# Kernel tuning notes

Hardware: AMD Instinct MI355X
Metric: run time of the kernel (lower is better)

The kernel has to match this reference:

```python
import jax, jax.numpy as jnp
import numpy as np

B, N, F_IN, H, E, C = 64, 1024, 128, 128, 1048576, 6
RATIO = 0.5
N1 = int(N * RATIO)        # nodes per graph after pool1 = 512
N2 = int(N1 * RATIO)       # nodes per graph after pool2 = 256


def setup_inputs() -> dict:
    key = jax.random.key(0)
    ks = jax.random.split(key, 14)
    x = jax.random.normal(ks[0], (B * N, F_IN), jnp.float32)
    # edges constrained within each graph (uniform graph size N)
    src = jax.random.randint(ks[1], (E,), 0, B * N, dtype=jnp.int32)
    dst = (src // N) * N + jax.random.randint(ks[2], (E,), 0, N, dtype=jnp.int32)
    edge_index = jnp.stack([src, dst]).astype(jnp.int64)
    batch = jnp.repeat(jnp.arange(B, dtype=jnp.int64), N)

    def lin(k, i, o):
        return (jax.random.normal(k, (i, o), jnp.float32) / np.sqrt(i)).astype(jnp.float32)

    W1 = lin(ks[3], F_IN, H); b1 = jnp.zeros((H,), jnp.float32)
    ws1 = jax.random.normal(ks[4], (H,), jnp.float32) / np.sqrt(H)
    W2 = lin(ks[5], H, H); b2 = jnp.zeros((H,), jnp.float32)
    ws2 = jax.random.normal(ks[6], (H,), jnp.float32) / np.sqrt(H)
    W3 = lin(ks[7], H, H); b3 = jnp.zeros((H,), jnp.float32)
    ws3 = jax.random.normal(ks[8], (H,), jnp.float32) / np.sqrt(H)
    L1w = lin(ks[9], 2 * H, H); L1b = jnp.zeros((H,), jnp.float32)
    L2w = lin(ks[10], H, H // 2); L2b = jnp.zeros((H // 2,), jnp.float32)
    L3w = lin(ks[11], H // 2, C); L3b = jnp.zeros((C,), jnp.float32)
    return dict(x=x, edge_index=edge_index, batch=batch,
                W1=W1, b1=b1, ws1=ws1, W2=W2, b2=b2, ws2=ws2, W3=W3, b3=b3, ws3=ws3,
                L1w=L1w, L1b=L1b, L2w=L2w, L2b=L2b, L3w=L3w, L3b=L3b)


def gcn_conv(x, src, dst, emask, W, b, ws, n_nodes):
    # GCNConv with self-loops: out_i = sum_j m_ij h_j / sqrt(d_i d_j) + h_i / d_i, d = deg+1
    h = x @ W
    deg = jax.ops.segment_sum(emask, dst, num_segments=n_nodes) + 1.0
    norm = emask / jnp.sqrt(deg[src] * deg[dst])                 # [E]
    agg = jax.ops.segment_sum(h[src] * norm[:, None], dst, num_segments=n_nodes)
    out = agg + h / deg[:, None] + b
    score = out @ ws                                             # [n] attention score
    return out, score


def att_pool(x, score, src, dst, emask, n_per_graph):
    # top-k node selection per graph (uniform sizes -> static shapes)
    k = int(n_per_graph * RATIO)
    vals, idx = jax.lax.top_k(score.reshape(B, n_per_graph), k)  # [B, k]
    gidx = (idx + (jnp.arange(B) * n_per_graph)[:, None]).reshape(-1)
    x_new = x[gidx] * jnp.tanh(vals.reshape(-1))[:, None]
    # remap old node ids -> new compact ids; drop edges touching removed nodes
    newpos = jnp.full((B * n_per_graph,), -1, jnp.int32).at[gidx].set(
        jnp.arange(B * k, dtype=jnp.int32))
    nsrc = newpos[src]; ndst = newpos[dst]
    nmask = emask * (nsrc >= 0) * (ndst >= 0)
    return x_new, jnp.maximum(nsrc, 0), jnp.maximum(ndst, 0), nmask, k


def readout(h, bvec, n_per_graph):
    gmp = jax.ops.segment_max(h, bvec, num_segments=B)
    gap = jax.ops.segment_sum(h, bvec, num_segments=B) / n_per_graph
    return jnp.concatenate([gmp, gap], axis=1)                   # [B, 2H]


def reference(x, edge_index, batch, W1, b1, ws1, W2, b2, ws2, W3, b3, ws3,
              L1w, L1b, L2w, L2b, L3w, L3b):
    src = edge_index[0].astype(jnp.int32)
    dst = edge_index[1].astype(jnp.int32)
    emask = jnp.ones((E,), x.dtype)

    h, s = gcn_conv(x, src, dst, emask, W1, b1, ws1, B * N)
    h = jax.nn.relu(h)
    h, src, dst, emask, k1 = att_pool(h, s, src, dst, emask, N)
    b1v = jnp.repeat(jnp.arange(B), k1)
    x1 = readout(h, b1v, float(k1))

    h, s = gcn_conv(h, src, dst, emask, W2, b2, ws2, B * k1)
    h = jax.nn.relu(h)
    h, src, dst, emask, k2 = att_pool(h, s, src, dst, emask, k1)
    b2v = jnp.repeat(jnp.arange(B), k2)
    x2 = readout(h, b2v, float(k2))

    h, s = gcn_conv(h, src, dst, emask, W3, b3, ws3, B * k2)
    h = jax.nn.relu(h)
    x3 = readout(h, b2v, float(k2))

    z = jax.nn.relu(x1) + jax.nn.relu(x2) + jax.nn.relu(x3)
    z = jax.nn.relu(z @ L1w + L1b)
    z = jax.nn.relu(z @ L2w + L2b)
    return jax.nn.log_softmax(z @ L3w + L3b, axis=-1)
```

## Files before the change

kernel.cpp:

```cpp
#include <hip/hip_runtime.h>
#include <math.h>

#define E_TOT 1048576
#define NB    64
#define HD    128
#define NN1   65536
#define NN2   32768
#define NN3   16384
#define CAP   18432
#define WST   140
#define PSTR  64

__global__ void probe_kernel(const int* __restrict__ ei, int* __restrict__ flag,
                             int* __restrict__ gcur) {
    int t = threadIdx.x;
    if (t < 64) gcur[t] = 0;
    if (blockIdx.x == 0 && t == 0) {
        int w = 1;
        for (int i = 1; i < 64; i += 2) if (ei[i] != 0) { w = 0; break; }
        *flag = w;
    }
}

__global__ __launch_bounds__(256) void bin_pack_kernel(const int* __restrict__ ei,
                                                       const int* __restrict__ wflag,
                                                       int* __restrict__ bins,
                                                       int* __restrict__ gcur) {
    __shared__ int hist[64];
    __shared__ int base[64];
    __shared__ int gpos[64];
    __shared__ int stage[4096];
    const int t = threadIdx.x;
    const int wide = *wflag;
    const int e0 = blockIdx.x * 4096;
    const int2* ei2 = (const int2*)ei;

    int pk[16];
    #pragma unroll
    for (int j = 0; j < 16; ++j) {
        int e = e0 + j * 256 + t;
        int s, d;
        if (wide) { s = ei2[e].x; d = ei2[E_TOT + e].x; }
        else      { s = ei[e];    d = ei[E_TOT + e]; }
        int g = d >> 10;
        pk[j] = (g << 20) | ((d & 1023) << 10) | (s & 1023);
    }
    if (t < 64) hist[t] = 0;
    __syncthreads();
    #pragma unroll
    for (int j = 0; j < 16; ++j) atomicAdd(&hist[pk[j] >> 20], 1);
    __syncthreads();
    if (t < 64) {
        int v = hist[t];
        int inc = v;
        #pragma unroll
        for (int d = 1; d < 64; d <<= 1) { int u = __shfl_up(inc, d); if (t >= d) inc += u; }
        base[t] = inc - v;
        gpos[t] = atomicAdd(&gcur[t], v);
    }
    __syncthreads();
    if (t < 64) hist[t] = base[t];
    __syncthreads();
    #pragma unroll
    for (int j = 0; j < 16; ++j) {
        int p = atomicAdd(&hist[pk[j] >> 20], 1);
        stage[p] = pk[j];
    }
    __syncthreads();
    #pragma unroll
    for (int j = 0; j < 16; ++j) {
        int i = j * 256 + t;
        int v = stage[i];
        int g = v >> 20;
        int dst = gpos[g] + (i - base[g]);
        if (dst < CAP) bins[g * CAP + dst] = v;
    }
}

__global__ __launch_bounds__(1024) void graph_csr_kernel(const int* __restrict__ bins,
                                                         const int* __restrict__ gcur,
                                                         int2* __restrict__ off2,
                                                         float* __restrict__ rs,
                                                         int* __restrict__ csr) {
    __shared__ int deg[1024];
    __shared__ int cur[1024];
    __shared__ int wsum[16];
    __shared__ int ebase_s;
    const int g = blockIdx.x, t = threadIdx.x;
    const int lane = t & 63, wv = t >> 6;

    if (t < 64) {
        int v = gcur[t];
        int inc = v;
        #pragma unroll
        for (int d = 1; d < 64; d <<= 1) { int u = __shfl_up(inc, d); if (t >= d) inc += u; }
        if (t == g) ebase_s = inc - v;
    }
    deg[t] = 0;
    __syncthreads();
    const int cnt = gcur[g];
    const int ebase = ebase_s;
    const int* bin = bins + g * CAP;

    for (int i = t; i < cnt; i += 1024)
        atomicAdd(&deg[(bin[i] >> 10) & 1023], 1);
    __syncthreads();

    int dv = deg[t];
    int inc = dv;
    #pragma unroll
    for (int d = 1; d < 64; d <<= 1) { int u = __shfl_up(inc, d); if (lane >= d) inc += u; }
    if (lane == 63) wsum[wv] = inc;
    __syncthreads();
    if (t < 16) {
        int v = wsum[t];
        int inc2 = v;
        #pragma unroll
        for (int d = 1; d < 16; d <<= 1) { int u = __shfl_up(inc2, d); if (t >= d) inc2 += u; }
        wsum[t] = inc2 - v;
    }
    __syncthreads();
    int ex = inc - dv + wsum[wv];
    int beg = ebase + ex;
    off2[g * 1024 + t] = make_int2(beg, beg + dv);
    rs[g * 1024 + t]   = rsqrtf((float)(dv + 1));
    cur[t] = ex;
    __syncthreads();

    for (int i = t; i < cnt; i += 1024) {
        int v = bin[i];
        int p = atomicAdd(&cur[(v >> 10) & 1023], 1);
        csr[ebase + p] = (g << 10) + (v & 1023);
    }
}

__global__ __launch_bounds__(256) void csr_build_kernel(const int2* __restrict__ old_off2,
                                                        const int* __restrict__ old_deg,
                                                        const int* __restrict__ old_csr,
                                                        const int* __restrict__ map,
                                                        const int* __restrict__ sel,
                                                        int* __restrict__ new_csr,
                                                        int* __restrict__ deg,
                                                        float* __restrict__ rs, int nnew) {
    int wid  = (blockIdx.x * blockDim.x + threadIdx.x) >> 6;
    int lane = threadIdx.x & 63;
    if (wid >= nnew) return;
    int old = sel[wid];
    int beg, end;
    if (old_off2) { int2 oe = old_off2[old]; beg = oe.x; end = oe.y; }
    else          { beg = old * PSTR; end = beg + old_deg[old]; }
    int out = wid * PSTR;
    int total = 0;
    for (int base = beg; base < end; base += 64) {
        int i = base + lane;
        int ns = -1;
        if (i < end) ns = map[old_csr[i]];
        unsigned long long b = __ballot(ns >= 0);
        int pos = __popcll(b & ((1ULL << lane) - 1));
        if (ns >= 0 && total + pos < PSTR) new_csr[out + total + pos] = ns;
        total += __popcll(b);
    }
    if (total > PSTR) total = PSTR;
    if (lane == 0) {
        deg[wid] = total;
        rs[wid]  = rsqrtf((float)(total + 1));
    }
}

__global__ __launch_bounds__(256) void gemm_tiled_kernel(const float* __restrict__ X,
                                                         const float* __restrict__ W,
                                                         float* __restrict__ Y) {
    __shared__ float sXT[2][16][128];
    __shared__ float sW[2][16][WST];
    const int t = threadIdx.x;
    const long long row0 = (long long)blockIdx.x * 128;
    const int r0 = (t >> 4) << 3;
    const int c0 = (t & 15) << 3;
    const int wofs = c0 + ((c0 >> 5) << 2);
    const int lm  = t >> 1;
    const int lk  = (t & 1) << 3;
    const int wk  = t >> 4;
    const int wc8 = (t & 15) << 3;
    const int wpos = wc8 + ((wc8 >> 5) << 2);

    float acc[8][8];
    #pragma unroll
    for (int i = 0; i < 8; ++i)
        #pragma unroll
        for (int j = 0; j < 8; ++j) acc[i][j] = 0.f;

    {
        float4 xa = *(const float4*)(X + (row0 + lm) * 128 + lk);
        float4 xb = *(const float4*)(X + (row0 + lm) * 128 + lk + 4);
        float4 wa = *(const float4*)(W + wk * 128 + wc8);
        float4 wb = *(const float4*)(W + wk * 128 + wc8 + 4);
        sXT[0][lk + 0][lm] = xa.x; sXT[0][lk + 1][lm] = xa.y;
        sXT[0][lk + 2][lm] = xa.z; sXT[0][lk + 3][lm] = xa.w;
        sXT[0][lk + 4][lm] = xb.x; sXT[0][lk + 5][lm] = xb.y;
        sXT[0][lk + 6][lm] = xb.z; sXT[0][lk + 7][lm] = xb.w;
        *(float4*)&sW[0][wk][wpos]     = wa;
        *(float4*)&sW[0][wk][wpos + 4] = wb;
    }
    int cur = 0;
    for (int k0 = 0; k0 < 128; k0 += 16) {
        __syncthreads();
        const bool hasNext = (k0 + 16) < 128;
        float4 nxa, nxb, nwa, nwb;
        if (hasNext) {
            nxa = *(const float4*)(X + (row0 + lm) * 128 + k0 + 16 + lk);
            nxb = *(const float4*)(X + (row0 + lm) * 128 + k0 + 16 + lk + 4);
            nwa = *(const float4*)(W + (k0 + 16 + wk) * 128 + wc8);
            nwb = *(const float4*)(W + (k0 + 16 + wk) * 128 + wc8 + 4);
        }
        #pragma unroll
        for (int kk = 0; kk < 16; ++kk) {
            float4 xa = *(const float4*)&sXT[cur][kk][r0];
            float4 xb = *(const float4*)&sXT[cur][kk][r0 + 4];
            float4 wa = *(const float4*)&sW[cur][kk][wofs];
            float4 wb = *(const float4*)&sW[cur][kk][wofs + 4];
            float xr[8]  = {xa.x, xa.y, xa.z, xa.w, xb.x, xb.y, xb.z, xb.w};
            float wcv[8] = {wa.x, wa.y, wa.z, wa.w, wb.x, wb.y, wb.z, wb.w};
            #pragma unroll
            for (int i = 0; i < 8; ++i)
                #pragma unroll
                for (int j = 0; j < 8; ++j)
                    acc[i][j] = fmaf(xr[i], wcv[j], acc[i][j]);
        }
        if (hasNext) {
            int nxt = cur ^ 1;
            sXT[nxt][lk + 0][lm] = nxa.x; sXT[nxt][lk + 1][lm] = nxa.y;
            sXT[nxt][lk + 2][lm] = nxa.z; sXT[nxt][lk + 3][lm] = nxa.w;
            sXT[nxt][lk + 4][lm] = nxb.x; sXT[nxt][lk + 5][lm] = nxb.y;
            sXT[nxt][lk + 6][lm] = nxb.z; sXT[nxt][lk + 7][lm] = nxb.w;
            *(float4*)&sW[nxt][wk][wpos]     = nwa;
            *(float4*)&sW[nxt][wk][wpos + 4] = nwb;
            cur = nxt;
        }
    }

    #pragma unroll
    for (int i = 0; i < 8; ++i) {
        float* yp = Y + (row0 + r0 + i) * 128 + c0;
        float4 o0; o0.x = acc[i][0]; o0.y = acc[i][1]; o0.z = acc[i][2]; o0.w = acc[i][3];
        float4 o1; o1.x = acc[i][4]; o1.y = acc[i][5]; o1.z = acc[i][6]; o1.w = acc[i][7];
        *(float4*)yp       = o0;
        *(float4*)(yp + 4) = o1;
    }
}

__global__ __launch_bounds__(256) void gemm_gather_kernel(const float* __restrict__ H,
                                                          const int* __restrict__ sel,
                                                          const float* __restrict__ scal,
                                                          const float* __restrict__ W,
                                                          float* __restrict__ Y) {
    __shared__ float sXT[2][16][128];
    __shared__ float sW[2][16][WST];
    const int t = threadIdx.x;
    const long long row0 = (long long)blockIdx.x * 128;
    const int r0 = (t >> 4) << 3;
    const int c0 = (t & 15) << 3;
    const int wofs = c0 + ((c0 >> 5) << 2);
    const int lm  = t >> 1;
    const int lk  = (t & 1) << 3;
    const int wk  = t >> 4;
    const int wc8 = (t & 15) << 3;
    const int wpos = wc8 + ((wc8 >> 5) << 2);

    const float* xrow = H + (long long)sel[row0 + lm] * 128;
    const float  sc   = scal[row0 + lm];

    float acc[8][8];
    #pragma unroll
    for (int i = 0; i < 8; ++i)
        #pragma unroll
        for (int j = 0; j < 8; ++j) acc[i][j] = 0.f;

    {
        float4 xa = *(const float4*)(xrow + lk);
        float4 xb = *(const float4*)(xrow + lk + 4);
        float4 wa = *(const float4*)(W + wk * 128 + wc8);
        float4 wb = *(const float4*)(W + wk * 128 + wc8 + 4);
        sXT[0][lk + 0][lm] = xa.x * sc; sXT[0][lk + 1][lm] = xa.y * sc;
        sXT[0][lk + 2][lm] = xa.z * sc; sXT[0][lk + 3][lm] = xa.w * sc;
        sXT[0][lk + 4][lm] = xb.x * sc; sXT[0][lk + 5][lm] = xb.y * sc;
        sXT[0][lk + 6][lm] = xb.z * sc; sXT[0][lk + 7][lm] = xb.w * sc;
        *(float4*)&sW[0][wk][wpos]     = wa;
        *(float4*)&sW[0][wk][wpos + 4] = wb;
    }
    int cur = 0;
    for (int k0 = 0; k0 < 128; k0 += 16) {
        __syncthreads();
        const bool hasNext = (k0 + 16) < 128;
        float4 nxa, nxb, nwa, nwb;
        if (hasNext) {
            nxa = *(const float4*)(xrow + k0 + 16 + lk);
            nxb = *(const float4*)(xrow + k0 + 16 + lk + 4);
            nwa = *(const float4*)(W + (k0 + 16 + wk) * 128 + wc8);
            nwb = *(const float4*)(W + (k0 + 16 + wk) * 128 + wc8 + 4);
        }
        #pragma unroll
        for (int kk = 0; kk < 16; ++kk) {
            float4 xa = *(const float4*)&sXT[cur][kk][r0];
            float4 xb = *(const float4*)&sXT[cur][kk][r0 + 4];
            float4 wa = *(const float4*)&sW[cur][kk][wofs];
            float4 wb = *(const float4*)&sW[cur][kk][wofs + 4];
            float xr[8]  = {xa.x, xa.y, xa.z, xa.w, xb.x, xb.y, xb.z, xb.w};
            float wcv[8] = {wa.x, wa.y, wa.z, wa.w, wb.x, wb.y, wb.z, wb.w};
            #pragma unroll
            for (int i = 0; i < 8; ++i)
                #pragma unroll
                for (int j = 0; j < 8; ++j)
                    acc[i][j] = fmaf(xr[i], wcv[j], acc[i][j]);
        }
        if (hasNext) {
            int nxt = cur ^ 1;
            sXT[nxt][lk + 0][lm] = nxa.x * sc; sXT[nxt][lk + 1][lm] = nxa.y * sc;
            sXT[nxt][lk + 2][lm] = nxa.z * sc; sXT[nxt][lk + 3][lm] = nxa.w * sc;
            sXT[nxt][lk + 4][lm] = nxb.x * sc; sXT[nxt][lk + 5][lm] = nxb.y * sc;
            sXT[nxt][lk + 6][lm] = nxb.z * sc; sXT[nxt][lk + 7][lm] = nxb.w * sc;
            *(float4*)&sW[nxt][wk][wpos]     = nwa;
            *(float4*)&sW[nxt][wk][wpos + 4] = nwb;
            cur = nxt;
        }
    }

    #pragma unroll
    for (int i = 0; i < 8; ++i) {
        float* yp = Y + (row0 + r0 + i) * 128 + c0;
        float4 o0; o0.x = acc[i][0]; o0.y = acc[i][1]; o0.z = acc[i][2]; o0.w = acc[i][3];
        float4 o1; o1.x = acc[i][4]; o1.y = acc[i][5]; o1.z = acc[i][6]; o1.w = acc[i][7];
        *(float4*)yp       = o0;
        *(float4*)(yp + 4) = o1;
    }
}

__global__ __launch_bounds__(256) void agg_kernel(const float* __restrict__ h,
                                                  const int* __restrict__ csr,
                                                  const int2* __restrict__ off2,
                                                  const int* __restrict__ degp,
                                                  const float* __restrict__ rs,
                                                  const float* __restrict__ bias,
                                                  const float* __restrict__ ws,
                                                  float* __restrict__ hrelu,
                                                  float* __restrict__ score,
                                                  int npg, int lbshift, int padded) {
    const int lane = threadIdx.x & 63;
    const int wvb  = threadIdx.x >> 6;
    const int half = lane >> 5;
    const int li   = lane & 31;
    int b   = blockIdx.x;
    int xcd = b & 7;
    int i   = b >> 3;
    int gi  = i >> lbshift;
    int lb  = i & ((1 << lbshift) - 1);
    int g   = xcd + (gi << 3);
    int v   = g * npg + (lb << 3) + (wvb << 1) + half;

    int beg, end;
    if (padded) { beg = v * PSTR; end = beg + degp[v]; }
    else        { int2 oe = off2[v]; beg = oe.x; end = oe.y; }
    float rv = rs[v];
    const float4* h4 = (const float4*)h;
    float ax = 0.f, ay = 0.f, az = 0.f, aw = 0.f;

    for (int base = beg; base < end; base += 32) {
        int idx = base + li;
        int sv = (idx < end) ? csr[idx] : 0;
        int m = end - base; if (m > 32) m = 32;
        int j = 0;
        for (; j + 8 <= m; j += 8) {
            int s0 = __shfl(sv, j,     32);
            int s1 = __shfl(sv, j + 1, 32);
            int s2 = __shfl(sv, j + 2, 32);
            int s3 = __shfl(sv, j + 3, 32);
            int s4 = __shfl(sv, j + 4, 32);
            int s5 = __shfl(sv, j + 5, 32);
            int s6 = __shfl(sv, j + 6, 32);
            int s7 = __shfl(sv, j + 7, 32);
            float n0 = rs[s0] * rv, n1 = rs[s1] * rv, n2 = rs[s2] * rv, n3 = rs[s3] * rv;
            float n4 = rs[s4] * rv, n5 = rs[s5] * rv, n6 = rs[s6] * rv, n7 = rs[s7] * rv;
            float4 v0 = h4[(long long)s0 * 32 + li];
            float4 v1 = h4[(long long)s1 * 32 + li];
            float4 v2 = h4[(long long)s2 * 32 + li];
            float4 v3 = h4[(long long)s3 * 32 + li];
            float4 v4 = h4[(long long)s4 * 32 + li];
            float4 v5 = h4[(long long)s5 * 32 + li];
            float4 v6 = h4[(long long)s6 * 32 + li];
            float4 v7 = h4[(long long)s7 * 32 + li];
            ax = fmaf(v0.x, n0, ax); ay = fmaf(v0.y, n0, ay); az = fmaf(v0.z, n0, az); aw = fmaf(v0.w, n0, aw);
            ax = fmaf(v1.x, n1, ax); ay = fmaf(v1.y, n1, ay); az = fmaf(v1.z, n1, az); aw = fmaf(v1.w, n1, aw);
            ax = fmaf(v2.x, n2, ax); ay = fmaf(v2.y, n2, ay); az = fmaf(v2.z, n2, az); aw = fmaf(v2.w, n2, aw);
            ax = fmaf(v3.x, n3, ax); ay = fmaf(v3.y, n3, ay); az = fmaf(v3.z, n3, az); aw = fmaf(v3.w, n3, aw);
            ax = fmaf(v4.x, n4, ax); ay = fmaf(v4.y, n4, ay); az = fmaf(v4.z, n4, az); aw = fmaf(v4.w, n4, aw);
            ax = fmaf(v5.x, n5, ax); ay = fmaf(v5.y, n5, ay); az = fmaf(v5.z, n5, az); aw = fmaf(v5.w, n5, aw);
            ax = fmaf(v6.x, n6, ax); ay = fmaf(v6.y, n6, ay); az = fmaf(v6.z, n6, az); aw = fmaf(v6.w, n6, aw);
            ax = fmaf(v7.x, n7, ax); ay = fmaf(v7.y, n7, ay); az = fmaf(v7.z, n7, az); aw = fmaf(v7.w, n7, aw);
        }
        for (; j < m; ++j) {
            int s = __shfl(sv, j, 32);
            float n = rs[s] * rv;
            float4 vv = h4[(long long)s * 32 + li];
            ax = fmaf(vv.x, n, ax); ay = fmaf(vv.y, n, ay);
            az = fmaf(vv.z, n, az); aw = fmaf(vv.w, n, aw);
        }
    }

    float4 hv = h4[(long long)v * 32 + li];
    float inv = rv * rv;
    float4 bb = ((const float4*)bias)[li];
    float4 ww = ((const float4*)ws)[li];
    float o0 = ax + hv.x * inv + bb.x;
    float o1 = ay + hv.y * inv + bb.y;
    float o2 = az + hv.z * inv + bb.z;
    float o3 = aw + hv.w * inv + bb.w;

    float pa = o0 * ww.x + o1 * ww.y;
    float pb = o2 * ww.z + o3 * ww.w;
    #pragma unroll
    for (int dd = 16; dd; dd >>= 1) {
        pa += __shfl_xor(pa, dd, 32);
        pb += __shfl_xor(pb, dd, 32);
    }
    float p = pa + pb;
    if (li == 0) score[v] = p;

    float4 o;
    o.x = fmaxf(o0, 0.f); o.y = fmaxf(o1, 0.f);
    o.z = fmaxf(o2, 0.f); o.w = fmaxf(o3, 0.f);
    ((float4*)hrelu)[(long long)v * 32 + li] = o;
}

__global__ __launch_bounds__(1024) void topk_kernel(const float* __restrict__ score,
                                                    int* __restrict__ newpos,
                                                    int* __restrict__ sel,
                                                    float* __restrict__ scale,
                                                    int n, int k) {
    __shared__ float key[1024];
    __shared__ int   kid[1024];
    int g = blockIdx.x, t = threadIdx.x;
    key[t] = score[g * n + t];
    kid[t] = t;
    __syncthreads();
    for (int kk = 2; kk <= n; kk <<= 1) {
        for (int j = kk >> 1; j > 0; j >>= 1) {
            int ixj = t ^ j;
            if (ixj > t) {
                bool dir = ((t & kk) == 0);
                float a = key[t], b = key[ixj];
                if ((a < b) == dir) {
                    key[t] = b; key[ixj] = a;
                    int tmp = kid[t]; kid[t] = kid[ixj]; kid[ixj] = tmp;
                }
            }
            __syncthreads();
        }
    }
    int old = g * n + kid[t];
    if (t < k) {
        int nid = g * k + t;
        newpos[old] = nid;
        sel[nid]    = old;
        scale[nid]  = tanhf(key[t]);
    } else {
        newpos[old] = -1;
    }
}

__global__ __launch_bounds__(128) void readout_part_kernel(const float* __restrict__ h,
                                                           float* __restrict__ part, int npg) {
    int b = blockIdx.x;
    int g = b >> 3, c = b & 7;
    int f = threadIdx.x;
    int chunk = npg >> 3;
    const float* base = h + ((long long)g * npg + (long long)c * chunk) * 128;
    float m = -INFINITY, s = 0.f;
    for (int n = 0; n < chunk; ++n) {
        float v = base[n * 128 + f];
        m = fmaxf(m, v);
        s += v;
    }
    part[(size_t)b * 256 + f]       = m;
    part[(size_t)b * 256 + 128 + f] = s;
}

__global__ __launch_bounds__(128) void readout_gpart_kernel(const float* __restrict__ h,
                                                            const int* __restrict__ sel,
                                                            const float* __restrict__ scal,
                                                            float* __restrict__ part, int npg) {
    int b = blockIdx.x;
    int g = b >> 3, c = b & 7;
    int f = threadIdx.x;
    int chunk = npg >> 3;
    int i0 = g * npg + c * chunk;
    float m = -INFINITY, s = 0.f;
    for (int n = 0; n < chunk; ++n) {
        int idx = i0 + n;
        float v = h[(long long)sel[idx] * 128 + f] * scal[idx];
        m = fmaxf(m, v);
        s += v;
    }
    part[(size_t)b * 256 + f]       = m;
    part[(size_t)b * 256 + 128 + f] = s;
}

__global__ __launch_bounds__(128) void mlp_kernel(const float* __restrict__ part1,
                                                  const float* __restrict__ part2,
                                                  const float* __restrict__ part3,
                                                  const float* __restrict__ L1w,
                                                  const float* __restrict__ L1b,
                                                  const float* __restrict__ L2w,
                                                  const float* __restrict__ L2b,
                                                  const float* __restrict__ L3w,
                                                  const float* __restrict__ L3b,
                                                  float* __restrict__ out) {
    __shared__ float z[256], z1[128], z2[64], z3[6];
    int g = blockIdx.x, t = threadIdx.x;
    float m1 = -INFINITY, s1 = 0.f, m2 = -INFINITY, s2 = 0.f, m3 = -INFINITY, s3 = 0.f;
    #pragma unroll
    for (int c = 0; c < 8; ++c) {
        size_t o = (size_t)(g * 8 + c) * 256;
        m1 = fmaxf(m1, part1[o + t]); s1 += part1[o + 128 + t];
        m2 = fmaxf(m2, part2[o + t]); s2 += part2[o + 128 + t];
        m3 = fmaxf(m3, part3[o + t]); s3 += part3[o + 128 + t];
    }
    z[t]       = fmaxf(m1, 0.f) + fmaxf(m2, 0.f) + fmaxf(m3, 0.f);
    z[t + 128] = fmaxf(s1 / 512.f, 0.f) + fmaxf(s2 / 256.f, 0.f) + fmaxf(s3 / 256.f, 0.f);
    __syncthreads();
    float a = L1b[t];
    for (int i = 0; i < 256; ++i) a += z[i] * L1w[i * 128 + t];
    z1[t] = fmaxf(a, 0.f);
    __syncthreads();
    if (t < 64) {
        float b = L2b[t];
        for (int i = 0; i < 128; ++i) b += z1[i] * L2w[i * 64 + t];
        z2[t] = fmaxf(b, 0.f);
    }
    __syncthreads();
    if (t < 6) {
        float c = L3b[t];
        for (int i = 0; i < 64; ++i) c += z2[i] * L3w[i * 6 + t];
        z3[t] = c;
    }
    __syncthreads();
    if (t == 0) {
        float m = z3[0];
        for (int i = 1; i < 6; ++i) m = fmaxf(m, z3[i]);
        float s = 0.f;
        for (int i = 0; i < 6; ++i) s += expf(z3[i] - m);
        float ls = m + logf(s);
        for (int i = 0; i < 6; ++i) out[g * 6 + i] = z3[i] - ls;
    }
}

extern "C" void kernel_launch(void* const* d_in, const int* in_sizes, int n_in,
                              void* d_out, int out_size, void* d_ws, size_t ws_size,
                              hipStream_t stream) {
    const float* x    = (const float*)d_in[0];
    const int*   ei   = (const int*)d_in[1];
    const float* W1   = (const float*)d_in[3];
    const float* b1   = (const float*)d_in[4];
    const float* ws1  = (const float*)d_in[5];
    const float* W2   = (const float*)d_in[6];
    const float* b2   = (const float*)d_in[7];
    const float* ws2  = (const float*)d_in[8];
    const float* W3   = (const float*)d_in[9];
    const float* b3   = (const float*)d_in[10];
    const float* ws3  = (const float*)d_in[11];
    const float* L1w  = (const float*)d_in[12];
    const float* L1b  = (const float*)d_in[13];
    const float* L2w  = (const float*)d_in[14];
    const float* L2b  = (const float*)d_in[15];
    const float* L3w  = (const float*)d_in[16];
    const float* L3b  = (const float*)d_in[17];
    float* out = (float*)d_out;

    char* w = (char*)d_ws;
    auto alloc = [&](size_t nbytes) { char* p = w; w += (nbytes + 255) & ~(size_t)255; return p; };
    float* A     = (float*)alloc((size_t)NN1 * 128 * 4);
    float* Bf    = (float*)alloc((size_t)NN1 * 128 * 4);
    float* P1    = (float*)alloc((size_t)NN2 * 128 * 4);
    float* P2    = (float*)alloc((size_t)NN3 * 128 * 4);
    int*   csrA  = (int*)alloc((size_t)E_TOT * 4);
    int*   degA  = (int*)alloc((size_t)NN2 * 4);
    int*   degB  = (int*)alloc((size_t)NN3 * 4);
    int2*  off2A = (int2*)alloc((size_t)NN1 * 8);
    float* rs    = (float*)alloc((size_t)NN1 * 4);
    int*   np1   = (int*)alloc((size_t)NN1 * 4);
    int*   np2   = (int*)alloc((size_t)NN2 * 4);
    int*   sel   = (int*)alloc((size_t)NN2 * 4);
    float* scal  = (float*)alloc((size_t)NN2 * 4);
    float* score = (float*)alloc((size_t)NN1 * 4);
    float* part1 = (float*)alloc((size_t)NB * 8 * 256 * 4);
    float* part2 = (float*)alloc((size_t)NB * 8 * 256 * 4);
    float* part3 = (float*)alloc((size_t)NB * 8 * 256 * 4);
    int*   gcur  = (int*)alloc(64 * 4);
    int*   flag  = (int*)alloc(256);

    int* bins = (int*)P2;
    int* csrB = (int*)P1;

    probe_kernel<<<1, 64, 0, stream>>>(ei, flag, gcur);

    bin_pack_kernel<<<E_TOT / 4096, 256, 0, stream>>>(ei, flag, bins, gcur);
    graph_csr_kernel<<<NB, 1024, 0, stream>>>(bins, gcur, off2A, rs, csrA);
    gemm_tiled_kernel<<<NN1 / 128, 256, 0, stream>>>(x, W1, A);
    agg_kernel<<<NN1 / 8, 256, 0, stream>>>(A, csrA, off2A, nullptr, rs, b1, ws1,
                                            Bf, score, 1024, 7, 0);
    topk_kernel<<<NB, 1024, 0, stream>>>(score, np1, sel, scal, 1024, 512);
    readout_gpart_kernel<<<NB * 8, 128, 0, stream>>>(Bf, sel, scal, part1, 512);

    csr_build_kernel<<<NN2 / 4, 256, 0, stream>>>(off2A, nullptr, csrA, np1, sel,
                                                  csrB, degA, rs, NN2);
    gemm_gather_kernel<<<NN2 / 128, 256, 0, stream>>>(Bf, sel, scal, W2, A);
    agg_kernel<<<NN2 / 8, 256, 0, stream>>>(A, csrB, nullptr, degA, rs, b2, ws2,
                                            Bf, score, 512, 6, 1);
    topk_kernel<<<NB, 512, 0, stream>>>(score, np2, sel, scal, 512, 256);
    readout_gpart_kernel<<<NB * 8, 128, 0, stream>>>(Bf, sel, scal, part2, 256);

    csr_build_kernel<<<NN3 / 4, 256, 0, stream>>>(nullptr, degA, csrB, np2, sel,
                                                  csrA, degB, rs, NN3);
    gemm_gather_kernel<<<NN3 / 128, 256, 0, stream>>>(Bf, sel, scal, W3, A);
    agg_kernel<<<NN3 / 8, 256, 0, stream>>>(A, csrA, nullptr, degB, rs, b3, ws3,
                                            Bf, score, 256, 5, 1);
    readout_part_kernel<<<NB * 8, 128, 0, stream>>>(Bf, part3, 256);

    mlp_kernel<<<NB, 128, 0, stream>>>(part1, part2, part3, L1w, L1b, L2w, L2b,
                                       L3w, L3b, out);
}
```

Before: 359.9 us.

## Store precomputed edge norms alongside CSR sources and add specialized first-layer aggregation

The first-layer CSR becomes an int2 array that pairs each source index with its precomputed normalization rsqrt(deg_s)*rsqrt(deg_d). A new aggregation kernel for layer 1 reads both values with one load and shuffles them across lanes, so it no longer gathers rs per edge. Unlike the old path it also handles remainders with masked fixed-size batches. In exchange the CSR doubles in size and graph construction writes more, and csr_build now reads the source indices with a stride of 2.

```diff
diff --git a/kernel.cpp b/kernel.cpp
--- a/kernel.cpp
+++ b/kernel.cpp
@@ -12,9 +12,9 @@
 #define PSTR  64
 
 __global__ void probe_kernel(const int* __restrict__ ei, int* __restrict__ flag,
-                             int* __restrict__ gcur) {
+                             int* __restrict__ gcur, int2* __restrict__ csr2) {
     int t = threadIdx.x;
-    if (t < 64) gcur[t] = 0;
+    if (t < 64) { gcur[t] = 0; csr2[E_TOT + t] = make_int2(0, 0); }
     if (blockIdx.x == 0 && t == 0) {
         int w = 1;
         for (int i = 1; i < 64; i += 2) if (ei[i] != 0) { w = 0; break; }
@@ -81,11 +81,12 @@
                                                          const int* __restrict__ gcur,
                                                          int2* __restrict__ off2,
                                                          float* __restrict__ rs,
-                                                         int* __restrict__ csr) {
-    __shared__ int deg[1024];
-    __shared__ int cur[1024];
-    __shared__ int wsum[16];
-    __shared__ int ebase_s;
+                                                         int2* __restrict__ csr2) {
+    __shared__ int   deg[1024];
+    __shared__ int   cur[1024];
+    __shared__ float rsl[1024];
+    __shared__ int   wsum[16];
+    __shared__ int   ebase_s;
     const int g = blockIdx.x, t = threadIdx.x;
     const int lane = t & 63, wv = t >> 6;
 
@@ -123,20 +124,25 @@
     int ex = inc - dv + wsum[wv];
     int beg = ebase + ex;
     off2[g * 1024 + t] = make_int2(beg, beg + dv);
-    rs[g * 1024 + t]   = rsqrtf((float)(dv + 1));
+    float rv = rsqrtf((float)(dv + 1));
+    rs[g * 1024 + t] = rv;
+    rsl[t] = rv;
     cur[t] = ex;
     __syncthreads();
 
     for (int i = t; i < cnt; i += 1024) {
         int v = bin[i];
-        int p = atomicAdd(&cur[(v >> 10) & 1023], 1);
-        csr[ebase + p] = (g << 10) + (v & 1023);
+        int s = v & 1023;
+        int d = (v >> 10) & 1023;
+        int p = atomicAdd(&cur[d], 1);
+        csr2[ebase + p] = make_int2((g << 10) + s, __float_as_int(rsl[s] * rsl[d]));
     }
 }
 
 __global__ __launch_bounds__(256) void csr_build_kernel(const int2* __restrict__ old_off2,
                                                         const int* __restrict__ old_deg,
                                                         const int* __restrict__ old_csr,
+                                                        int old_stride,
                                                         const int* __restrict__ map,
                                                         const int* __restrict__ sel,
                                                         int* __restrict__ new_csr,
@@ -154,7 +160,7 @@
     for (int base = beg; base < end; base += 64) {
         int i = base + lane;
         int ns = -1;
-        if (i < end) ns = map[old_csr[i]];
+        if (i < end) ns = map[old_csr[i * old_stride]];
         unsigned long long b = __ballot(ns >= 0);
         int pos = __popcll(b & ((1ULL << lane) - 1));
         if (ns >= 0 && total + pos < PSTR) new_csr[out + total + pos] = ns;
@@ -332,6 +338,108 @@
         *(float4*)yp       = o0;
         *(float4*)(yp + 4) = o1;
     }
+}
+
+__global__ __launch_bounds__(256) void aggn_kernel(const float* __restrict__ h,
+                                                   const int2* __restrict__ csr2,
+                                                   const int2* __restrict__ off2,
+                                                   const float* __restrict__ rs,
+                                                   const float* __restrict__ bias,
+                                                   const float* __restrict__ ws,
+                                                   float* __restrict__ hrelu,
+                                                   float* __restrict__ score,
+                                                   int npg, int lbshift) {
+    const int lane = threadIdx.x & 63;
+    const int wvb  = threadIdx.x >> 6;
+    const int half = lane >> 5;
+    const int li   = lane & 31;
+    int b   = blockIdx.x;
+    int xcd = b & 7;
+    int i   = b >> 3;
+    int gi  = i >> lbshift;
+    int lb  = i & ((1 << lbshift) - 1);
+    int g   = xcd + (gi << 3);
+    int v   = g * npg + (lb << 3) + (wvb << 1) + half;
+
+    int2 oe = off2[v];
+    int beg = oe.x, end = oe.y;
+    float rv = rs[v];
+    const char* hb = (const char*)h;
+    const int lofs = li << 4;
+    float ax = 0.f, ay = 0.f, az = 0.f, aw = 0.f;
+
+#define AGG_L(K) \
+    int s##K = __shfl(sv.x, j + K, 32); \
+    float n##K = __int_as_float(__shfl(sv.y, j + K, 32)); \
+    float4 e##K = *(const float4*)(hb + ((s##K << 9) + lofs));
+#define AGG_LM(K) \
+    int s##K = __shfl(sv.x, j + K, 32); \
+    float nr##K = __int_as_float(__shfl(sv.y, j + K, 32)); \
+    float n##K = (j + K < m) ? nr##K : 0.f; \
+    float4 e##K = *(const float4*)(hb + ((s##K << 9) + lofs));
+#define AGG_F(K) \
+    ax = fmaf(e##K.x, n##K, ax); ay = fmaf(e##K.y, n##K, ay); \
+    az = fmaf(e##K.z, n##K, az); aw = fmaf(e##K.w, n##K, aw);
+
+    for (int base = beg; base < end; base += 32) {
+        int idx = base + li;
+        int2 sv = csr2[idx];
+        int m = end - base; if (m > 32) m = 32;
+        int j = 0;
+        for (; j + 16 <= m; j += 16) {
+            AGG_L(0)  AGG_L(1)  AGG_L(2)  AGG_L(3)
+            AGG_L(4)  AGG_L(5)  AGG_L(6)  AGG_L(7)
+            AGG_L(8)  AGG_L(9)  AGG_L(10) AGG_L(11)
+            AGG_L(12) AGG_L(13) AGG_L(14) AGG_L(15)
+            AGG_F(0)  AGG_F(1)  AGG_F(2)  AGG_F(3)
+            AGG_F(4)  AGG_F(5)  AGG_F(6)  AGG_F(7)
+            AGG_F(8)  AGG_F(9)  AGG_F(10) AGG_F(11)
+            AGG_F(12) AGG_F(13) AGG_F(14) AGG_F(15)
+        }
+        int rem = m - j;
+        if (rem > 8) {
+            AGG_LM(0)  AGG_LM(1)  AGG_LM(2)  AGG_LM(3)
+            AGG_LM(4)  AGG_LM(5)  AGG_LM(6)  AGG_LM(7)
+            AGG_LM(8)  AGG_LM(9)  AGG_LM(10) AGG_LM(11)
+            AGG_LM(12) AGG_LM(13) AGG_LM(14) AGG_LM(15)
+            AGG_F(0)  AGG_F(1)  AGG_F(2)  AGG_F(3)
+            AGG_F(4)  AGG_F(5)  AGG_F(6)  AGG_F(7)
+            AGG_F(8)  AGG_F(9)  AGG_F(10) AGG_F(11)
+            AGG_F(12) AGG_F(13) AGG_F(14) AGG_F(15)
+        } else if (rem > 0) {
+            AGG_LM(0) AGG_LM(1) AGG_LM(2) AGG_LM(3)
+            AGG_LM(4) AGG_LM(5) AGG_LM(6) AGG_LM(7)
+            AGG_F(0) AGG_F(1) AGG_F(2) AGG_F(3)
+            AGG_F(4) AGG_F(5) AGG_F(6) AGG_F(7)
+        }
+    }
+#undef AGG_L
+#undef AGG_LM
+#undef AGG_F
+
+    float4 hv = *(const float4*)(hb + ((v << 9) + lofs));
+    float inv = rv * rv;
+    float4 bb = ((const float4*)bias)[li];
+    float4 ww = ((const float4*)ws)[li];
+    float o0 = ax + hv.x * inv + bb.x;
+    float o1 = ay + hv.y * inv + bb.y;
+    float o2 = az + hv.z * inv + bb.z;
+    float o3 = aw + hv.w * inv + bb.w;
+
+    float pa = o0 * ww.x + o1 * ww.y;
+    float pb = o2 * ww.z + o3 * ww.w;
+    #pragma unroll
+    for (int dd = 16; dd; dd >>= 1) {
+        pa += __shfl_xor(pa, dd, 32);
+        pb += __shfl_xor(pb, dd, 32);
+    }
+    float p = pa + pb;
+    if (li == 0) score[v] = p;
+
+    float4 o;
+    o.x = fmaxf(o0, 0.f); o.y = fmaxf(o1, 0.f);
+    o.z = fmaxf(o2, 0.f); o.w = fmaxf(o3, 0.f);
+    *(float4*)((char*)hrelu + ((v << 9) + lofs)) = o;
 }
 
 __global__ __launch_bounds__(256) void agg_kernel(const float* __restrict__ h,
@@ -580,7 +688,7 @@
     float* Bf    = (float*)alloc((size_t)NN1 * 128 * 4);
     float* P1    = (float*)alloc((size_t)NN2 * 128 * 4);
     float* P2    = (float*)alloc((size_t)NN3 * 128 * 4);
-    int*   csrA  = (int*)alloc((size_t)E_TOT * 4);
+    int2*  csr2  = (int2*)alloc((size_t)(E_TOT + 64) * 8);
     int*   degA  = (int*)alloc((size_t)NN2 * 4);
     int*   degB  = (int*)alloc((size_t)NN3 * 4);
     int2*  off2A = (int2*)alloc((size_t)NN1 * 8);
@@ -598,29 +706,30 @@
 
     int* bins = (int*)P2;
     int* csrB = (int*)P1;
-
-    probe_kernel<<<1, 64, 0, stream>>>(ei, flag, gcur);
+    int* csrC = (int*)csr2;
+
+    probe_kernel<<<1, 64, 0, stream>>>(ei, flag, gcur, csr2);
 
     bin_pack_kernel<<<E_TOT / 4096, 256, 0, stream>>>(ei, flag, bins, gcur);
-    graph_csr_kernel<<<NB, 1024, 0, stream>>>(bins, gcur, off2A, rs, csrA);
+    graph_csr_kernel<<<NB, 1024, 0, stream>>>(bins, gcur, off2A, rs, csr2);
     gemm_tiled_kernel<<<NN1 / 128, 256, 0, stream>>>(x, W1, A);
-    agg_kernel<<<NN1 / 8, 256, 0, stream>>>(A, csrA, off2A, nullptr, rs, b1, ws1,
-                                            Bf, score, 1024, 7, 0);
+    aggn_kernel<<<NN1 / 8, 256, 0, stream>>>(A, csr2, off2A, rs, b1, ws1,
+                                             Bf, score, 1024, 7);
     topk_kernel<<<NB, 1024, 0, stream>>>(score, np1, sel, scal, 1024, 512);
     readout_gpart_kernel<<<NB * 8, 128, 0, stream>>>(Bf, sel, scal, part1, 512);
 
-    csr_build_kernel<<<NN2 / 4, 256, 0, stream>>>(off2A, nullptr, csrA, np1, sel,
-                                                  csrB, degA, rs, NN2);
+    csr_build_kernel<<<NN2 / 4, 256, 0, stream>>>(off2A, nullptr, (const int*)csr2, 2,
+                                                  np1, sel, csrB, degA, rs, NN2);
     gemm_gather_kernel<<<NN2 / 128, 256, 0, stream>>>(Bf, sel, scal, W2, A);
     agg_kernel<<<NN2 / 8, 256, 0, stream>>>(A, csrB, nullptr, degA, rs, b2, ws2,
                                             Bf, score, 512, 6, 1);
     topk_kernel<<<NB, 512, 0, stream>>>(score, np2, sel, scal, 512, 256);
     readout_gpart_kernel<<<NB * 8, 128, 0, stream>>>(Bf, sel, scal, part2, 256);
 
-    csr_build_kernel<<<NN3 / 4, 256, 0, stream>>>(nullptr, degA, csrB, np2, sel,
-                                                  csrA, degB, rs, NN3);
+    csr_build_kernel<<<NN3 / 4, 256, 0, stream>>>(nullptr, degA, csrB, 1,
+                                                  np2, sel, csrC, degB, rs, NN3);
     gemm_gather_kernel<<<NN3 / 128, 256, 0, stream>>>(Bf, sel, scal, W3, A);
-    agg_kernel<<<NN3 / 8, 256, 0, stream>>>(A, csrA, nullptr, degB, rs, b3, ws3,
+    agg_kernel<<<NN3 / 8, 256, 0, stream>>>(A, csrC, nullptr, degB, rs, b3, ws3,
                                             Bf, score, 256, 5, 1);
     readout_part_kernel<<<NB * 8, 128, 0, stream>>>(Bf, part3, 256);
 
```

After: 358.0 us. About the same (-0.5%).

## Aggregate first GCN layer from LDS-staged per-graph features with precomputed edge norms

Applied to the files above, without the earlier changes.

Adds an agg_lds_kernel for layer 1. Each block stages one graph's 1024-node by 32-feature slice of h in LDS and gathers neighbor rows from shared memory instead of global memory. The CSR now stores (src, norm) pairs precomputed in graph_csr_kernel, so the per-edge rsqrt product is not recomputed. Score partials are written per feature chunk to a buffer that topk_kernel reduces, which removes a cross-block reduction. The cost is doubled CSR storage, strided index reads in the next csr_build, a large LDS footprint that limits occupancy, and a padded tail of csr2 to cover 8-wide over-reads.

```diff
diff --git a/kernel.cpp b/kernel.cpp
--- a/kernel.cpp
+++ b/kernel.cpp
@@ -12,9 +12,9 @@
 #define PSTR  64
 
 __global__ void probe_kernel(const int* __restrict__ ei, int* __restrict__ flag,
-                             int* __restrict__ gcur) {
+                             int* __restrict__ gcur, int2* __restrict__ csr2) {
     int t = threadIdx.x;
-    if (t < 64) gcur[t] = 0;
+    if (t < 64) { gcur[t] = 0; csr2[E_TOT + t] = make_int2(0, 0); }
     if (blockIdx.x == 0 && t == 0) {
         int w = 1;
         for (int i = 1; i < 64; i += 2) if (ei[i] != 0) { w = 0; break; }
@@ -81,11 +81,12 @@
                                                          const int* __restrict__ gcur,
                                                          int2* __restrict__ off2,
                                                          float* __restrict__ rs,
-                                                         int* __restrict__ csr) {
-    __shared__ int deg[1024];
-    __shared__ int cur[1024];
-    __shared__ int wsum[16];
-    __shared__ int ebase_s;
+                                                         int2* __restrict__ csr2) {
+    __shared__ int   deg[1024];
+    __shared__ int   cur[1024];
+    __shared__ float rsl[1024];
+    __shared__ int   wsum[16];
+    __shared__ int   ebase_s;
     const int g = blockIdx.x, t = threadIdx.x;
     const int lane = t & 63, wv = t >> 6;
 
@@ -123,20 +124,25 @@
     int ex = inc - dv + wsum[wv];
     int beg = ebase + ex;
     off2[g * 1024 + t] = make_int2(beg, beg + dv);
-    rs[g * 1024 + t]   = rsqrtf((float)(dv + 1));
+    float rv = rsqrtf((float)(dv + 1));
+    rs[g * 1024 + t] = rv;
+    rsl[t] = rv;
     cur[t] = ex;
     __syncthreads();
 
     for (int i = t; i < cnt; i += 1024) {
         int v = bin[i];
-        int p = atomicAdd(&cur[(v >> 10) & 1023], 1);
-        csr[ebase + p] = (g << 10) + (v & 1023);
+        int s = v & 1023;
+        int d = (v >> 10) & 1023;
+        int p = atomicAdd(&cur[d], 1);
+        csr2[ebase + p] = make_int2((g << 10) + s, __float_as_int(rsl[s] * rsl[d]));
     }
 }
 
 __global__ __launch_bounds__(256) void csr_build_kernel(const int2* __restrict__ old_off2,
                                                         const int* __restrict__ old_deg,
                                                         const int* __restrict__ old_csr,
+                                                        int old_stride,
                                                         const int* __restrict__ map,
                                                         const int* __restrict__ sel,
                                                         int* __restrict__ new_csr,
@@ -154,7 +160,7 @@
     for (int base = beg; base < end; base += 64) {
         int i = base + lane;
         int ns = -1;
-        if (i < end) ns = map[old_csr[i]];
+        if (i < end) ns = map[old_csr[i * old_stride]];
         unsigned long long b = __ballot(ns >= 0);
         int pos = __popcll(b & ((1ULL << lane) - 1));
         if (ns >= 0 && total + pos < PSTR) new_csr[out + total + pos] = ns;
@@ -331,6 +337,77 @@
         float4 o1; o1.x = acc[i][4]; o1.y = acc[i][5]; o1.z = acc[i][6]; o1.w = acc[i][7];
         *(float4*)yp       = o0;
         *(float4*)(yp + 4) = o1;
+    }
+}
+
+__global__ __launch_bounds__(1024) void agg_lds_kernel(const float* __restrict__ h,
+                                                       const int2* __restrict__ csr2,
+                                                       const int2* __restrict__ off2,
+                                                       const float* __restrict__ rs,
+                                                       const float* __restrict__ bias,
+                                                       const float* __restrict__ ws,
+                                                       float* __restrict__ hrelu,
+                                                       float* __restrict__ P) {
+    __shared__ float sh[1024 * 36];
+    const int t  = threadIdx.x;
+    const int g  = blockIdx.x & 63;
+    const int fc = blockIdx.x >> 6;
+    const int nbase = g << 10;
+    const float* hg = h + (size_t)nbase * 128 + fc * 32;
+
+    #pragma unroll
+    for (int it = 0; it < 8; ++it) {
+        int i = it * 1024 + t;
+        int r = i >> 3, p = i & 7;
+        float4 v4 = *(const float4*)(hg + (size_t)r * 128 + p * 4);
+        *(float4*)&sh[r * 36 + p * 4] = v4;
+    }
+    __syncthreads();
+
+    const int q  = t & 7;
+    const int wv = t >> 6;
+    const int ns = (t >> 3) & 7;
+    const int qb = q << 2;
+
+    float4 bb = *(const float4*)(bias + fc * 32 + qb);
+    float4 ww = *(const float4*)(ws   + fc * 32 + qb);
+
+    for (int pass = 0; pass < 8; ++pass) {
+        int lv = wv * 64 + pass * 8 + ns;
+        int v  = nbase + lv;
+        int2 oe = off2[v];
+        int beg = oe.x, end = oe.y;
+        float rv = rs[v];
+        float a0 = 0.f, a1 = 0.f, a2 = 0.f, a3 = 0.f;
+
+        for (int eb = beg; eb < end; eb += 8) {
+            int2 er[8];
+            #pragma unroll
+            for (int j = 0; j < 8; ++j) er[j] = csr2[eb + j];
+            #pragma unroll
+            for (int j = 0; j < 8; ++j) {
+                float nj = (eb + j < end) ? __int_as_float(er[j].y) : 0.f;
+                const float4 e = *(const float4*)&sh[(er[j].x & 1023) * 36 + qb];
+                a0 = fmaf(e.x, nj, a0); a1 = fmaf(e.y, nj, a1);
+                a2 = fmaf(e.z, nj, a2); a3 = fmaf(e.w, nj, a3);
+            }
+        }
+
+        float4 hv = *(const float4*)&sh[lv * 36 + qb];
+        float inv = rv * rv;
+        float o0 = a0 + hv.x * inv + bb.x;
+        float o1 = a1 + hv.y * inv + bb.y;
+        float o2 = a2 + hv.z * inv + bb.z;
+        float o3 = a3 + hv.w * inv + bb.w;
+
+        float pa = o0 * ww.x + o1 * ww.y;
+        float pb = o2 * ww.z + o3 * ww.w;
+        *(float2*)(P + (size_t)v * 64 + (fc * 8 + q) * 2) = make_float2(pa, pb);
+
+        float4 o;
+        o.x = fmaxf(o0, 0.f); o.y = fmaxf(o1, 0.f);
+        o.z = fmaxf(o2, 0.f); o.w = fmaxf(o3, 0.f);
+        *(float4*)(hrelu + (size_t)v * 128 + fc * 32 + qb) = o;
     }
 }
 
@@ -431,6 +508,7 @@
 }
 
 __global__ __launch_bounds__(1024) void topk_kernel(const float* __restrict__ score,
+                                                    const float* __restrict__ P,
                                                     int* __restrict__ newpos,
                                                     int* __restrict__ sel,
                                                     float* __restrict__ scale,
@@ -438,7 +516,32 @@
     __shared__ float key[1024];
     __shared__ int   kid[1024];
     int g = blockIdx.x, t = threadIdx.x;
-    key[t] = score[g * n + t];
+    float sc;
+    if (P) {
+        const float* buf = P + (size_t)(g * n + t) * 64;
+        float a[32], b[32];
+        #pragma unroll
+        for (int i2 = 0; i2 < 16; ++i2) {
+            float4 v4 = *(const float4*)(buf + i2 * 4);
+            a[i2 * 2]     = v4.x; b[i2 * 2]     = v4.y;
+            a[i2 * 2 + 1] = v4.z; b[i2 * 2 + 1] = v4.w;
+        }
+        float ua[16], ub[16];
+        #pragma unroll
+        for (int l = 0; l < 16; ++l) { ua[l] = a[l] + a[l + 16]; ub[l] = b[l] + b[l + 16]; }
+        float va[8], vb[8];
+        #pragma unroll
+        for (int l = 0; l < 8; ++l) { va[l] = ua[l] + ua[l + 8]; vb[l] = ub[l] + ub[l + 8]; }
+        float wa[4], wb[4];
+        #pragma unroll
+        for (int l = 0; l < 4; ++l) { wa[l] = va[l] + va[l + 4]; wb[l] = vb[l] + vb[l + 4]; }
+        float xa0 = wa[0] + wa[2], xa1 = wa[1] + wa[3];
+        float xb0 = wb[0] + wb[2], xb1 = wb[1] + wb[3];
+        sc = (xa0 + xa1) + (xb0 + xb1);
+    } else {
+        sc = score[g * n + t];
+    }
+    key[t] = sc;
     kid[t] = t;
     __syncthreads();
     for (int kk = 2; kk <= n; kk <<= 1) {
@@ -578,9 +681,9 @@
     auto alloc = [&](size_t nbytes) { char* p = w; w += (nbytes + 255) & ~(size_t)255; return p; };
     float* A     = (float*)alloc((size_t)NN1 * 128 * 4);
     float* Bf    = (float*)alloc((size_t)NN1 * 128 * 4);
-    float* P1    = (float*)alloc((size_t)NN2 * 128 * 4);
+    float* P1    = (float*)alloc((size_t)NN1 * 64 * 4);
     float* P2    = (float*)alloc((size_t)NN3 * 128 * 4);
-    int*   csrA  = (int*)alloc((size_t)E_TOT * 4);
+    int2*  csr2  = (int2*)alloc((size_t)(E_TOT + 64) * 8);
     int*   degA  = (int*)alloc((size_t)NN2 * 4);
     int*   degB  = (int*)alloc((size_t)NN3 * 4);
     int2*  off2A = (int2*)alloc((size_t)NN1 * 8);
@@ -596,31 +699,32 @@
     int*   gcur  = (int*)alloc(64 * 4);
     int*   flag  = (int*)alloc(256);
 
-    int* bins = (int*)P2;
-    int* csrB = (int*)P1;
-
-    probe_kernel<<<1, 64, 0, stream>>>(ei, flag, gcur);
+    int*   bins = (int*)P2;
+    float* Pp   = P1;
+    int*   csrB = (int*)P1;
+    int*   csrC = (int*)csr2;
+
+    probe_kernel<<<1, 64, 0, stream>>>(ei, flag, gcur, csr2);
 
     bin_pack_kernel<<<E_TOT / 4096, 256, 0, stream>>>(ei, flag, bins, gcur);
-    graph_csr_kernel<<<NB, 1024, 0, stream>>>(bins, gcur, off2A, rs, csrA);
+    graph_csr_kernel<<<NB, 1024, 0, stream>>>(bins, gcur, off2A, rs, csr2);
     gemm_tiled_kernel<<<NN1 / 128, 256, 0, stream>>>(x, W1, A);
-    agg_kernel<<<NN1 / 8, 256, 0, stream>>>(A, csrA, off2A, nullptr, rs, b1, ws1,
-                                            Bf, score, 1024, 7, 0);
-    topk_kernel<<<NB, 1024, 0, stream>>>(score, np1, sel, scal, 1024, 512);
+    agg_lds_kernel<<<256, 1024, 0, stream>>>(A, csr2, off2A, rs, b1, ws1, Bf, Pp);
+    topk_kernel<<<NB, 1024, 0, stream>>>(nullptr, Pp, np1, sel, scal, 1024, 512);
     readout_gpart_kernel<<<NB * 8, 128, 0, stream>>>(Bf, sel, scal, part1, 512);
 
-    csr_build_kernel<<<NN2 / 4, 256, 0, stream>>>(off2A, nullptr, csrA, np1, sel,
-                                                  csrB, degA, rs, NN2);
+    csr_build_kernel<<<NN2 / 4, 256, 0, stream>>>(off2A, nullptr, (const int*)csr2, 2,
+                                                  np1, sel, csrB, degA, rs, NN2);
     gemm_gather_kernel<<<NN2 / 128, 256, 0, stream>>>(Bf, sel, scal, W2, A);
     agg_kernel<<<NN2 / 8, 256, 0, stream>>>(A, csrB, nullptr, degA, rs, b2, ws2,
                                             Bf, score, 512, 6, 1);
-    topk_kernel<<<NB, 512, 0, stream>>>(score, np2, sel, scal, 512, 256);
+    topk_kernel<<<NB, 512, 0, stream>>>(score, nullptr, np2, sel, scal, 512, 256);
     readout_gpart_kernel<<<NB * 8, 128, 0, stream>>>(Bf, sel, scal, part2, 256);
 
-    csr_build_kernel<<<NN3 / 4, 256, 0, stream>>>(nullptr, degA, csrB, np2, sel,
-                                                  csrA, degB, rs, NN3);
+    csr_build_kernel<<<NN3 / 4, 256, 0, stream>>>(nullptr, degA, csrB, 1,
+                                                  np2, sel, csrC, degB, rs, NN3);
     gemm_gather_kernel<<<NN3 / 128, 256, 0, stream>>>(Bf, sel, scal, W3, A);
-    agg_kernel<<<NN3 / 8, 256, 0, stream>>>(A, csrA, nullptr, degB, rs, b3, ws3,
+    agg_kernel<<<NN3 / 8, 256, 0, stream>>>(A, csrC, nullptr, degB, rs, b3, ws3,
                                             Bf, score, 256, 5, 1);
     readout_part_kernel<<<NB * 8, 128, 0, stream>>>(Bf, part3, 256);
 
```

After: 364.1 us. Within noise of the previous version (+1.2%).
